# Optimization experiments

Hardware: AMD Instinct MI355X
Metric: run time of the kernel (lower is better)

Reference implementation:

```python
import jax, jax.numpy as jnp
import numpy as np

D_MODEL = 256
POOL = 3
SR = 2  # sampling_ratio
TEMP = 10000.0


def pos_grid(D, H, W):
    """2D sine-cos positional encoding, (D,H,W). pos_y channels first, pos_x second."""
    dq = D // 4
    dim_t = TEMP ** (2.0 * (jnp.arange(dq) // 2).astype(jnp.float32) / dq)

    def enc(coord):  # (L,) -> (L, 2*dq), interleaved sin/cos
        p = coord[:, None] / dim_t
        return jnp.stack([jnp.sin(p), jnp.cos(p)], axis=-1).reshape(coord.shape[0], -1)

    py = enc(jnp.linspace(0.0, 1.0, H))  # (H, 2dq)
    px = enc(jnp.linspace(0.0, 1.0, W))  # (W, 2dq)
    pos = jnp.concatenate([
        jnp.broadcast_to(py[:, None, :], (H, W, 2 * dq)),
        jnp.broadcast_to(px[None, :, :], (H, W, 2 * dq)),
    ], axis=-1)  # (H, W, D)
    return jnp.transpose(pos, (2, 0, 1))  # (D, H, W)


def proj_pos(x, Wp, bp):
    """1x1 conv projection to D then add 2D pos enc. x: (B,C,H,W) -> (B,D,H,W)."""
    y = jnp.einsum('bchw,dc->bdhw', x, Wp) + bp[None, :, None, None]
    return y + pos_grid(Wp.shape[0], x.shape[2], x.shape[3])[None]


def roi_align_mean(feat, bidx, boxes, scale):
    """torchvision roi_align (aligned=True, sampling_ratio=SR, output=POOLxPOOL)
    followed by mean over the pooled grid. feat (B,D,H,W), boxes (N,4) xyxy -> (N,D).
    Since every bin averages SR*SR samples, mean over bins == mean over all samples."""
    B, D, H, W = feat.shape
    f = jnp.transpose(feat, (0, 2, 3, 1))  # (B,H,W,D)
    x1 = boxes[:, 0] * scale - 0.5
    y1 = boxes[:, 1] * scale - 0.5
    x2 = boxes[:, 2] * scale - 0.5
    y2 = boxes[:, 3] * scale - 0.5
    bw = (x2 - x1) / POOL
    bh = (y2 - y1) / POOL
    # sample offsets within roi, in units of bin size: (POOL*SR,)
    off = (jnp.arange(POOL, dtype=jnp.float32)[:, None]
           + (jnp.arange(SR, dtype=jnp.float32)[None, :] + 0.5) / SR).reshape(-1)
    ys = y1[:, None] + bh[:, None] * off  # (N,S) with S = POOL*SR
    xs = x1[:, None] + bw[:, None] * off

    def coords(c, size):
        valid = (c >= -1.0) & (c <= size)
        c = jnp.clip(c, 0.0, None)
        cl = jnp.minimum(jnp.floor(c).astype(jnp.int32), size - 1)
        ch = jnp.minimum(cl + 1, size - 1)
        return cl, ch, c - cl, valid

    yl, yh, ly, vy = coords(ys, H)
    xl, xh, lx, vx = coords(xs, W)
    hy, hx = 1.0 - ly, 1.0 - lx

    def gather(yy, xx):  # -> (N,S,S,D)
        return f[bidx[:, None, None], yy[:, :, None], xx[:, None, :]]

    v = (hy[:, :, None, None] * hx[:, None, :, None] * gather(yl, xl)
         + hy[:, :, None, None] * lx[:, None, :, None] * gather(yl, xh)
         + ly[:, :, None, None] * hx[:, None, :, None] * gather(yh, xl)
         + ly[:, :, None, None] * lx[:, None, :, None] * gather(yh, xh))
    mask = (vy[:, :, None] & vx[:, None, :])[..., None]
    v = jnp.where(mask, v, 0.0)
    return v.mean(axis=(1, 2))  # (N, D)


def token_mlp(tok, ln_g, ln_b, W1, b1, W2, b2):
    m = tok.mean(-1, keepdims=True)
    var = jnp.mean((tok - m) ** 2, -1, keepdims=True)
    h = (tok - m) / jnp.sqrt(var + 1e-5) * ln_g + ln_b
    h = jax.nn.gelu(h @ W1.T + b1, approximate=False)  # torch nn.GELU default = exact
    return h @ W2.T + b2


def setup_inputs():
    key = jax.random.key(0)
    ks = jax.random.split(key, 16)
    B, K, D = 8, 100, D_MODEL
    p3 = jax.random.normal(ks[0], (B, 512, 128, 128), jnp.float32)
    p4 = jax.random.normal(ks[1], (B, 1024, 64, 64), jnp.float32)
    p5 = jax.random.normal(ks[2], (B, 2048, 32, 32), jnp.float32)
    # valid xyxy boxes inside a 1024x1024 frame
    x1 = jax.random.uniform(ks[3], (B, K, 1)) * 880.0
    y1 = jax.random.uniform(ks[4], (B, K, 1)) * 880.0
    bw = jax.random.uniform(ks[5], (B, K, 1)) * 128.0 + 8.0
    bh = jax.random.uniform(ks[6], (B, K, 1)) * 128.0 + 8.0
    boxes = jnp.concatenate([x1, y1, x1 + bw, y1 + bh], axis=-1)

    def lin(k, o, i):
        return (jax.random.normal(k, (o, i), jnp.float32) / np.sqrt(i)).astype(jnp.float32)

    return dict(
        p3=p3, p4=p4, p5=p5, boxes=boxes,
        W3=lin(ks[7], D, 512), b3=jnp.zeros((D,), jnp.float32),
        W4=lin(ks[8], D, 1024), b4=jnp.zeros((D,), jnp.float32),
        W5=lin(ks[9], D, 2048), b5=jnp.zeros((D,), jnp.float32),
        ln_g=jnp.ones((D,), jnp.float32), ln_b=jnp.zeros((D,), jnp.float32),
        W1=lin(ks[10], D, D), b1=jnp.zeros((D,), jnp.float32),
        W2=lin(ks[11], D, D), b2=jnp.zeros((D,), jnp.float32),
        input_w=1024, input_h=1024,
    )


def reference(p3, p4, p5, boxes, W3, b3, W4, b4, W5, b5, ln_g, ln_b, W1, b1, W2, b2, input_w, input_h):
    B, K = boxes.shape[0], boxes.shape[1]
    bidx = jnp.repeat(jnp.arange(B, dtype=jnp.int32), K)  # (B*K,)
    flat = boxes.reshape(-1, 4)
    tok = jnp.zeros((B * K, D_MODEL), jnp.float32)
    for feat, Wp, bp in ((p3, W3, b3), (p4, W4, b4), (p5, W5, b5)):
        y = proj_pos(feat, Wp, bp)
        s = min(y.shape[3] / (input_w + 1e-6), y.shape[2] / (input_h + 1e-6))
        tok = tok + roi_align_mean(y, bidx, flat, s)
    tok = token_mlp(tok, ln_g, ln_b, W1, b1, W2, b2)
    return tok.reshape(B, K, D_MODEL)
```

## Files before the change

### kernel.cpp

```cpp
#include <hip/hip_runtime.h>
#include <math.h>

#ifndef INT_MAX
#define INT_MAX 0x7fffffff
#endif


__device__ __forceinline__ float gelu_exact(float x) {
    return 0.5f * x * (1.0f + erff(x * 0.70710678118654752f));
}

__global__ __launch_bounds__(256)
void build_wt_kernel(const float* __restrict__ W3, const float* __restrict__ W4,
                     const float* __restrict__ W5, const float* __restrict__ W1,
                     const float* __restrict__ W2,
                     float* __restrict__ WT, float* __restrict__ W1T,
                     float* __restrict__ W2T)
{
    int k = blockIdx.x;
    int d = threadIdx.x;
    if (k < 512)       WT[(size_t)k * 256 + d]          = W3[(size_t)d * 512  + k];
    else if (k < 1536) WT[(size_t)k * 256 + d]          = W4[(size_t)d * 1024 + (k - 512)];
    else if (k < 3584) WT[(size_t)k * 256 + d]          = W5[(size_t)d * 2048 + (k - 1536)];
    else if (k < 3840) W1T[(size_t)(k - 3584) * 256 + d] = W1[(size_t)d * 256 + (k - 3584)];
    else               W2T[(size_t)(k - 3840) * 256 + d] = W2[(size_t)d * 256 + (k - 3840)];
}

__global__ __launch_bounds__(256)
void roi_setup_kernel(const float* __restrict__ boxes,
                      const float* __restrict__ b3, const float* __restrict__ b4,
                      const float* __restrict__ b5,
                      const int* __restrict__ iw_p, const int* __restrict__ ih_p,
                      float* __restrict__ WREC, float* __restrict__ P)
{
    const int n   = blockIdx.x;
    const int s   = blockIdx.y;
    const int tid = threadIdx.x;

    int H, W;
    const float* bp;
    if (s == 0)      { H = 128; W = 128; bp = b3; }
    else if (s == 1) { H = 64;  W = 64;  bp = b4; }
    else             { H = 32;  W = 32;  bp = b5; }

    __shared__ float wy[32];
    __shared__ float wx[48];
    __shared__ int   sh_r0, sh_rs, sh_x0, sh_nc;
    __shared__ float sh_syc, sh_sxc;

    if (tid < 32)                 wy[tid]      = 0.0f;
    if (tid >= 32 && tid < 80)    wx[tid - 32] = 0.0f;
    __syncthreads();

    const float scale = fminf((float)W / ((float)(*iw_p) + 1e-6f),
                              (float)H / ((float)(*ih_p) + 1e-6f));

    if (tid == 0) {
        float c1 = boxes[(size_t)n * 4 + 1] * scale - 0.5f;
        float c2 = boxes[(size_t)n * 4 + 3] * scale - 0.5f;
        float bs = (c2 - c1) / 3.0f;
        int   yls[6], yhs[6], vv[6];
        float lys[6];
        int r0 = INT_MAX; float cnt = 0.0f;
        #pragma unroll
        for (int i = 0; i < 6; ++i) {
            float off = 0.25f + 0.5f * (float)i;
            float ys  = c1 + bs * off;
            int v = (ys >= -1.0f) && (ys <= (float)H);
            float yc = fmaxf(ys, 0.0f);
            int yl = (int)floorf(yc); if (yl > H - 1) yl = H - 1;
            int yh = yl + 1;          if (yh > H - 1) yh = H - 1;
            float ly = yc - (float)yl;
            yls[i] = yl; yhs[i] = yh; lys[i] = ly; vv[i] = v;
            if (v) { r0 = min(r0, yl); cnt += 1.0f; }
        }
        if (r0 == INT_MAX) r0 = 0;
        int rmax = 0;
        #pragma unroll
        for (int i = 0; i < 6; ++i) if (vv[i]) {
            int a = min(yls[i] - r0, 31);
            int h = min(yhs[i] - r0, 31);
            wy[a] += 1.0f - lys[i];
            wy[h] += lys[i];
            rmax = max(rmax, h);
        }
        sh_r0 = r0; sh_rs = rmax + 1; sh_syc = cnt;
    }
    if (tid == 1) {
        float c1 = boxes[(size_t)n * 4 + 0] * scale - 0.5f;
        float c2 = boxes[(size_t)n * 4 + 2] * scale - 0.5f;
        float bs = (c2 - c1) / 3.0f;
        int   xls[6], xhs[6], vv[6];
        float lxs[6];
        int x0r = INT_MAX; float cnt = 0.0f;
        #pragma unroll
        for (int i = 0; i < 6; ++i) {
            float off = 0.25f + 0.5f * (float)i;
            float xs  = c1 + bs * off;
            int v = (xs >= -1.0f) && (xs <= (float)W);
            float xc = fmaxf(xs, 0.0f);
            int xl = (int)floorf(xc); if (xl > W - 1) xl = W - 1;
            int xh = xl + 1;          if (xh > W - 1) xh = W - 1;
            float lx = xc - (float)xl;
            xls[i] = xl; xhs[i] = xh; lxs[i] = lx; vv[i] = v;
            if (v) { x0r = min(x0r, xl); cnt += 1.0f; }
        }
        if (x0r == INT_MAX) x0r = 0;
        int x0 = x0r & ~15;
        int imax = 0;
        #pragma unroll
        for (int i = 0; i < 6; ++i) if (vv[i]) {
            int a = min(xls[i] - x0, 47);
            int h = min(xhs[i] - x0, 47);
            wx[a] += 1.0f - lxs[i];
            wx[h] += lxs[i];
            imax = max(imax, h);
        }
        int nc = imax / 16 + 1;
        int ncmax = (W - x0) >> 4;
        nc = min(nc, ncmax);
        sh_x0 = x0; sh_nc = max(nc, 1); sh_sxc = cnt;
    }
    __syncthreads();

    const int r0 = sh_r0, rs = sh_rs, x0 = sh_x0, nc = sh_nc;

    float* rec = &WREC[(size_t)(n * 3 + s) * 96];
    if (tid < 32)                 rec[tid]      = wy[tid];
    else if (tid < 80)            rec[tid]      = wx[tid - 32];
    else if (tid == 80)           rec[80]       = (float)r0;
    else if (tid == 81)           rec[81]       = (float)rs;
    else if (tid == 82)           rec[82]       = (float)x0;
    else if (tid == 83)           rec[83]       = (float)nc;
    else if (tid == 84)           rec[84]       = sh_syc;
    else if (tid == 85)           rec[85]       = sh_sxc;

    {
        const int d = tid;
        const float syc = sh_syc, sxc = sh_sxc;
        float val;
        if (d < 128) {
            int   t     = d >> 2;
            float invf  = expf(-(float)t * (logf(10000.0f) / 32.0f));
            float istep = 1.0f / (float)(H - 1);
            float sum = 0.0f;
            for (int r = 0; r < rs; ++r) {
                float w = wy[r];
                float ang = (float)(r0 + r) * istep * invf;
                float sn, cs; sincosf(ang, &sn, &cs);
                sum = fmaf(w, (d & 1) ? cs : sn, sum);
            }
            val = sxc * sum;
        } else {
            int   d2    = d - 128;
            int   t     = d2 >> 2;
            float invf  = expf(-(float)t * (logf(10000.0f) / 32.0f));
            float istep = 1.0f / (float)(W - 1);
            float sum = 0.0f;
            int nx = nc << 4;
            for (int j = 0; j < nx; ++j) {
                float w = wx[j];
                if (w != 0.0f) {
                    float ang = (float)(x0 + j) * istep * invf;
                    float sn, cs; sincosf(ang, &sn, &cs);
                    sum = fmaf(w, (d & 1) ? cs : sn, sum);
                }
            }
            val = syc * sum;
        }
        float cnt = syc * sxc;
        P[((size_t)n * 3 + s) * 256 + d] = (val + cnt * bp[d]) * (1.0f / 36.0f);
    }
}

__global__ __launch_bounds__(256)
void roi_gather_kernel(const float* __restrict__ p3, const float* __restrict__ p4,
                       const float* __restrict__ p5,
                       const float* __restrict__ WREC,
                       float* __restrict__ G, int K)
{
    const int yc  = blockIdx.x;
    const int n   = blockIdx.y;
    const int tid = threadIdx.x;

    int s, chunk;
    if (yc < 8)       { s = 0; chunk = yc; }
    else if (yc < 24) { s = 1; chunk = yc - 8; }
    else              { s = 2; chunk = yc - 24; }

    int C, H, W, koff;
    const float* feat;
    if (s == 0)      { C = 512;  H = 128; W = 128; koff = 0;    feat = p3; }
    else if (s == 1) { C = 1024; H = 64;  W = 64;  koff = 512;  feat = p4; }
    else             { C = 2048; H = 32;  W = 32;  koff = 1536; feat = p5; }
    const int HW = H * W;
    const int b  = n / K;

    __shared__ float sh[96];
    if (tid < 96) sh[tid] = WREC[(size_t)(n * 3 + s) * 96 + tid];
    __syncthreads();

    const int r0 = (int)sh[80];
    const int rs = (int)sh[81];
    const int x0 = (int)sh[82];
    const int nc = (int)sh[83];

    const int c    = chunk * 64 + (tid >> 2);
    const int slot = tid & 3;

    const float* fp = feat + (size_t)b * C * HW + (size_t)c * HW
                    + (size_t)r0 * W + x0 + slot * 4;

    float acc = 0.0f;
    for (int ch = 0; ch < nc; ++ch) {
        const float4 wxv = *(const float4*)&sh[32 + (ch << 4) + slot * 4];
        const float* a = fp + (ch << 4);
        float4 ra = make_float4(0.f, 0.f, 0.f, 0.f);
        int r = 0;
        for (; r + 4 <= rs; r += 4) {
            const float4 v0 = *(const float4*)(a + (size_t)(r + 0) * W);
            const float4 v1 = *(const float4*)(a + (size_t)(r + 1) * W);
            const float4 v2 = *(const float4*)(a + (size_t)(r + 2) * W);
            const float4 v3 = *(const float4*)(a + (size_t)(r + 3) * W);
            const float w0 = sh[r], w1 = sh[r + 1], w2 = sh[r + 2], w3 = sh[r + 3];
            ra.x = fmaf(w0, v0.x, ra.x); ra.y = fmaf(w0, v0.y, ra.y);
            ra.z = fmaf(w0, v0.z, ra.z); ra.w = fmaf(w0, v0.w, ra.w);
            ra.x = fmaf(w1, v1.x, ra.x); ra.y = fmaf(w1, v1.y, ra.y);
            ra.z = fmaf(w1, v1.z, ra.z); ra.w = fmaf(w1, v1.w, ra.w);
            ra.x = fmaf(w2, v2.x, ra.x); ra.y = fmaf(w2, v2.y, ra.y);
            ra.z = fmaf(w2, v2.z, ra.z); ra.w = fmaf(w2, v2.w, ra.w);
            ra.x = fmaf(w3, v3.x, ra.x); ra.y = fmaf(w3, v3.y, ra.y);
            ra.z = fmaf(w3, v3.z, ra.z); ra.w = fmaf(w3, v3.w, ra.w);
        }
        for (; r < rs; ++r) {
            const float4 v = *(const float4*)(a + (size_t)r * W);
            const float w = sh[r];
            ra.x = fmaf(w, v.x, ra.x); ra.y = fmaf(w, v.y, ra.y);
            ra.z = fmaf(w, v.z, ra.z); ra.w = fmaf(w, v.w, ra.w);
        }
        float d = ra.x * wxv.x + ra.y * wxv.y + ra.z * wxv.z + ra.w * wxv.w;
        acc += d;
    }
    acc += __shfl_xor(acc, 1, 4);
    acc += __shfl_xor(acc, 2, 4);
    if (slot == 0)
        G[(size_t)n * 3584 + koff + c] = acc * (1.0f / 36.0f);
}

__global__ __launch_bounds__(256)
void proj_gemm_kernel(const float* __restrict__ G, const float* __restrict__ WT,
                      float* __restrict__ part, int N)
{
    const int n0  = blockIdx.x * 8;
    const int kc  = blockIdx.y;
    const int tid = threadIdx.x;

    __shared__ float gl[8][128];
    float acc[8];
    #pragma unroll
    for (int t = 0; t < 8; ++t) acc[t] = 0.0f;

    const int kbase = kc * 512;
    const int lt  = tid >> 5;
    const int lc  = (tid & 31) * 4;

    for (int sub = 0; sub < 4; ++sub) {
        const float4 g4 = *(const float4*)&G[(size_t)(n0 + lt) * 3584 + kbase + sub * 128 + lc];
        *(float4*)&gl[lt][lc] = g4;
        __syncthreads();
        const float* wtp = &WT[(size_t)(kbase + sub * 128) * 256 + tid];
        #pragma unroll 4
        for (int k = 0; k < 128; ++k) {
            float w = wtp[(size_t)k * 256];
            #pragma unroll
            for (int t = 0; t < 8; ++t) acc[t] = fmaf(gl[t][k], w, acc[t]);
        }
        __syncthreads();
    }
    #pragma unroll
    for (int t = 0; t < 8; ++t)
        part[((size_t)kc * N + n0 + t) * 256 + tid] = acc[t];
}

__global__ __launch_bounds__(256)
void mlp_kernel(const float* __restrict__ part, const float* __restrict__ P,
                const float* __restrict__ lng, const float* __restrict__ lnb,
                const float* __restrict__ W1T, const float* __restrict__ b1,
                const float* __restrict__ W2T, const float* __restrict__ b2,
                float* __restrict__ out, int N)
{
    const int n0  = blockIdx.x * 8;
    const int tid = threadIdx.x;

    __shared__ float tokl[8][257];
    __shared__ float hl[8][257];
    __shared__ float mval[8], rstd[8];

    #pragma unroll
    for (int t = 0; t < 8; ++t) {
        const int n = n0 + t;
        float v = 0.0f;
        #pragma unroll
        for (int c = 0; c < 7; ++c) v += part[((size_t)c * N + n) * 256 + tid];
        #pragma unroll
        for (int s = 0; s < 3; ++s) v += P[((size_t)n * 3 + s) * 256 + tid];
        tokl[t][tid] = v;
    }
    __syncthreads();

    const int wv = tid >> 6, lane = tid & 63;
    for (int t = wv; t < 8; t += 4) {
        float x0 = tokl[t][lane], x1 = tokl[t][lane + 64];
        float x2 = tokl[t][lane + 128], x3 = tokl[t][lane + 192];
        float sm = x0 + x1 + x2 + x3;
        float sq = x0 * x0 + x1 * x1 + x2 * x2 + x3 * x3;
        #pragma unroll
        for (int o = 32; o; o >>= 1) { sm += __shfl_xor(sm, o); sq += __shfl_xor(sq, o); }
        if (lane == 0) {
            float m   = sm * (1.0f / 256.0f);
            float var = sq * (1.0f / 256.0f) - m * m;
            mval[t] = m;
            rstd[t] = rsqrtf(var + 1e-5f);
        }
    }
    __syncthreads();

    const float g = lng[tid], be = lnb[tid];
    #pragma unroll
    for (int t = 0; t < 8; ++t)
        hl[t][tid] = (tokl[t][tid] - mval[t]) * rstd[t] * g + be;
    __syncthreads();

    float acc[8];
    const float bb1 = b1[tid];
    #pragma unroll
    for (int t = 0; t < 8; ++t) acc[t] = bb1;
    for (int k = 0; k < 256; ++k) {
        float w = W1T[(size_t)k * 256 + tid];
        #pragma unroll
        for (int t = 0; t < 8; ++t) acc[t] = fmaf(hl[t][k], w, acc[t]);
    }
    __syncthreads();
    #pragma unroll
    for (int t = 0; t < 8; ++t) tokl[t][tid] = gelu_exact(acc[t]);
    __syncthreads();

    const float bb2 = b2[tid];
    #pragma unroll
    for (int t = 0; t < 8; ++t) acc[t] = bb2;
    for (int k = 0; k < 256; ++k) {
        float w = W2T[(size_t)k * 256 + tid];
        #pragma unroll
        for (int t = 0; t < 8; ++t) acc[t] = fmaf(tokl[t][k], w, acc[t]);
    }
    #pragma unroll
    for (int t = 0; t < 8; ++t)
        out[(size_t)(n0 + t) * 256 + tid] = acc[t];
}

extern "C" void kernel_launch(void* const* d_in, const int* in_sizes, int n_in,
                              void* d_out, int out_size, void* d_ws, size_t ws_size,
                              hipStream_t stream)
{
    const float* p3    = (const float*)d_in[0];
    const float* p4    = (const float*)d_in[1];
    const float* p5    = (const float*)d_in[2];
    const float* boxes = (const float*)d_in[3];
    const float* W3    = (const float*)d_in[4];
    const float* b3    = (const float*)d_in[5];
    const float* W4    = (const float*)d_in[6];
    const float* b4    = (const float*)d_in[7];
    const float* W5    = (const float*)d_in[8];
    const float* b5    = (const float*)d_in[9];
    const float* lng   = (const float*)d_in[10];
    const float* lnb   = (const float*)d_in[11];
    const float* W1    = (const float*)d_in[12];
    const float* b1    = (const float*)d_in[13];
    const float* W2    = (const float*)d_in[14];
    const float* b2    = (const float*)d_in[15];
    const int*   iw    = (const int*)d_in[16];
    const int*   ih    = (const int*)d_in[17];

    const int B = in_sizes[0] / (512 * 128 * 128);
    const int N = out_size / 256;
    const int K = N / B;

    float* G    = (float*)d_ws;
    float* P    = G + (size_t)N * 3584;
    float* WT   = P + (size_t)N * 3 * 256;
    float* W1T  = WT + (size_t)3584 * 256;
    float* W2T  = W1T + (size_t)256 * 256;
    float* part = W2T + (size_t)256 * 256;
    float* WREC = part + (size_t)7 * N * 256;

    float* out = (float*)d_out;

    build_wt_kernel<<<4096, 256, 0, stream>>>(W3, W4, W5, W1, W2, WT, W1T, W2T);
    roi_setup_kernel<<<dim3(N, 3), 256, 0, stream>>>(boxes, b3, b4, b5, iw, ih, WREC, P);
    roi_gather_kernel<<<dim3(56, N), 256, 0, stream>>>(p3, p4, p5, WREC, G, K);
    proj_gemm_kernel<<<dim3(N / 8, 7), 256, 0, stream>>>(G, WT, part, N);
    mlp_kernel<<<N / 8, 256, 0, stream>>>(part, P, lng, lnb, W1T, b1, W2T, b2, out, N);
}
```

Measured before the change: 269.7 us.

## Project full feature maps with fp16 MFMA before ROI sampling

Reorders the pipeline: each pyramid level is first projected to 256 channels with an fp16 MFMA GEMM over all pixels, and bilinear ROI sampling then runs on the compact fp16 projected maps. Positional encoding and bias are handled analytically in a setup kernel. This replaces the gather over wide 512–2048 channel inputs and the per-ROI projection GEMM with dense tensor-core work. It adds full-map compute and fp16 rounding, and falls back to the old path if the workspace is too small.

```diff
diff --git a/kernel.cpp b/kernel.cpp
--- a/kernel.cpp
+++ b/kernel.cpp
@@ -1,14 +1,421 @@
 #include <hip/hip_runtime.h>
+#include <hip/hip_fp16.h>
 #include <math.h>
 
 #ifndef INT_MAX
 #define INT_MAX 0x7fffffff
 #endif
 
+typedef __attribute__((ext_vector_type(8))) _Float16 f16x8;
+typedef __attribute__((ext_vector_type(4))) float   f32x4;
+
 
 __device__ __forceinline__ float gelu_exact(float x) {
     return 0.5f * x * (1.0f + erff(x * 0.70710678118654752f));
 }
+
+
+__global__ __launch_bounds__(256)
+void build_wt2_kernel(const float* __restrict__ W3, const float* __restrict__ W4,
+                      const float* __restrict__ W5, const float* __restrict__ W1,
+                      const float* __restrict__ W2,
+                      __half* __restrict__ WTD,
+                      float* __restrict__ W1T, float* __restrict__ W2T)
+{
+    const int k = blockIdx.x;
+    const int d = threadIdx.x;
+    if (k < 3584) {
+        const size_t i = (size_t)k * 256 + d;
+        float v;
+        if (i < 131072)       v = W3[i];
+        else if (i < 393216)  v = W4[i - 131072];
+        else                  v = W5[i - 393216];
+        WTD[i] = __float2half(v);
+    } else if (k < 3840) {
+        W1T[(size_t)(k - 3584) * 256 + d] = W1[(size_t)d * 256 + (k - 3584)];
+    } else {
+        W2T[(size_t)(k - 3840) * 256 + d] = W2[(size_t)d * 256 + (k - 3840)];
+    }
+}
+
+__global__ __launch_bounds__(256)
+void roi_setup2_kernel(const float* __restrict__ boxes,
+                       const float* __restrict__ b3, const float* __restrict__ b4,
+                       const float* __restrict__ b5,
+                       const int* __restrict__ iw_p, const int* __restrict__ ih_p,
+                       float* __restrict__ SREC, float* __restrict__ P)
+{
+    const int n   = blockIdx.x;
+    const int s   = blockIdx.y;
+    const int tid = threadIdx.x;
+
+    int H, W;
+    const float* bp;
+    if (s == 0)      { H = 128; W = 128; bp = b3; }
+    else if (s == 1) { H = 64;  W = 64;  bp = b4; }
+    else             { H = 32;  W = 32;  bp = b5; }
+
+    __shared__ float wy[32];
+    __shared__ float wx[48];
+    __shared__ int   sh_r0, sh_rs, sh_x0, sh_xs;
+    __shared__ float sh_syc, sh_sxc;
+
+    if (tid < 32)              wy[tid]      = 0.0f;
+    if (tid >= 32 && tid < 80) wx[tid - 32] = 0.0f;
+    __syncthreads();
+
+    const float scale = fminf((float)W / ((float)(*iw_p) + 1e-6f),
+                              (float)H / ((float)(*ih_p) + 1e-6f));
+    float* rec = &SREC[(size_t)(n * 3 + s) * 64];
+
+    if (tid == 0) {
+        float c1 = boxes[(size_t)n * 4 + 1] * scale - 0.5f;
+        float c2 = boxes[(size_t)n * 4 + 3] * scale - 0.5f;
+        float bs = (c2 - c1) / 3.0f;
+        int   yls[6], yhs[6], vv[6];
+        float lys[6];
+        int r0 = INT_MAX; float cnt = 0.0f;
+        #pragma unroll
+        for (int i = 0; i < 6; ++i) {
+            float off = 0.25f + 0.5f * (float)i;
+            float ys  = c1 + bs * off;
+            int v = (ys >= -1.0f) && (ys <= (float)H);
+            float yc = fmaxf(ys, 0.0f);
+            int yl = (int)floorf(yc); if (yl > H - 1) yl = H - 1;
+            int yh = yl + 1;          if (yh > H - 1) yh = H - 1;
+            float ly = yc - (float)yl;
+            yls[i] = yl; yhs[i] = yh; lys[i] = ly; vv[i] = v;
+            if (v) { r0 = min(r0, yl); cnt += 1.0f; }
+        }
+        if (r0 == INT_MAX) r0 = 0;
+        int rmax = 0;
+        #pragma unroll
+        for (int i = 0; i < 6; ++i) if (vv[i]) {
+            int a = min(yls[i] - r0, 31);
+            int h = min(yhs[i] - r0, 31);
+            wy[a] += 1.0f - lys[i];
+            wy[h] += lys[i];
+            rmax = max(rmax, h);
+        }
+        sh_r0 = r0; sh_rs = rmax + 1; sh_syc = cnt;
+        int cntn = 0;
+        for (int r = 0; r <= rmax && cntn < 12; ++r) {
+            if (wy[r] != 0.0f) {
+                rec[4 + cntn]  = (float)(r0 + r);
+                rec[16 + cntn] = wy[r];
+                ++cntn;
+            }
+        }
+        rec[0] = (float)cntn;
+        rec[2] = cnt;
+    }
+    if (tid == 1) {
+        float c1 = boxes[(size_t)n * 4 + 0] * scale - 0.5f;
+        float c2 = boxes[(size_t)n * 4 + 2] * scale - 0.5f;
+        float bs = (c2 - c1) / 3.0f;
+        int   xls[6], xhs[6], vv[6];
+        float lxs[6];
+        int x0r = INT_MAX; float cnt = 0.0f;
+        #pragma unroll
+        for (int i = 0; i < 6; ++i) {
+            float off = 0.25f + 0.5f * (float)i;
+            float xs  = c1 + bs * off;
+            int v = (xs >= -1.0f) && (xs <= (float)W);
+            float xc = fmaxf(xs, 0.0f);
+            int xl = (int)floorf(xc); if (xl > W - 1) xl = W - 1;
+            int xh = xl + 1;          if (xh > W - 1) xh = W - 1;
+            float lx = xc - (float)xl;
+            xls[i] = xl; xhs[i] = xh; lxs[i] = lx; vv[i] = v;
+            if (v) { x0r = min(x0r, xl); cnt += 1.0f; }
+        }
+        if (x0r == INT_MAX) x0r = 0;
+        int imax = 0;
+        #pragma unroll
+        for (int i = 0; i < 6; ++i) if (vv[i]) {
+            int a = min(xls[i] - x0r, 47);
+            int h = min(xhs[i] - x0r, 47);
+            wx[a] += 1.0f - lxs[i];
+            wx[h] += lxs[i];
+            imax = max(imax, h);
+        }
+        sh_x0 = x0r; sh_xs = imax + 1; sh_sxc = cnt;
+        int cntn = 0;
+        for (int j = 0; j <= imax && cntn < 12; ++j) {
+            if (wx[j] != 0.0f) {
+                rec[28 + cntn] = (float)(x0r + j);
+                rec[40 + cntn] = wx[j];
+                ++cntn;
+            }
+        }
+        rec[1] = (float)cntn;
+        rec[3] = cnt;
+    }
+    __syncthreads();
+
+    const int r0 = sh_r0, rs = sh_rs, x0 = sh_x0, xsr = sh_xs;
+
+    {
+        const int d = tid;
+        const float syc = sh_syc, sxc = sh_sxc;
+        float val;
+        if (d < 128) {
+            int   t     = d >> 2;
+            float invf  = expf(-(float)t * (logf(10000.0f) / 32.0f));
+            float istep = 1.0f / (float)(H - 1);
+            float sum = 0.0f;
+            for (int r = 0; r < rs; ++r) {
+                float w = wy[r];
+                if (w != 0.0f) {
+                    float ang = (float)(r0 + r) * istep * invf;
+                    float sn, cs; sincosf(ang, &sn, &cs);
+                    sum = fmaf(w, (d & 1) ? cs : sn, sum);
+                }
+            }
+            val = sxc * sum;
+        } else {
+            int   d2    = d - 128;
+            int   t     = d2 >> 2;
+            float invf  = expf(-(float)t * (logf(10000.0f) / 32.0f));
+            float istep = 1.0f / (float)(W - 1);
+            float sum = 0.0f;
+            for (int j = 0; j < xsr; ++j) {
+                float w = wx[j];
+                if (w != 0.0f) {
+                    float ang = (float)(x0 + j) * istep * invf;
+                    float sn, cs; sincosf(ang, &sn, &cs);
+                    sum = fmaf(w, (d & 1) ? cs : sn, sum);
+                }
+            }
+            val = syc * sum;
+        }
+        float cnt = syc * sxc;
+        P[((size_t)n * 3 + s) * 256 + d] = (val + cnt * bp[d]) * (1.0f / 36.0f);
+    }
+}
+
+__global__ __launch_bounds__(256, 2)
+void proj_kernel(const float* __restrict__ p3, const float* __restrict__ p4,
+                 const float* __restrict__ p5,
+                 const __half* __restrict__ wt3, const __half* __restrict__ wt4,
+                 const __half* __restrict__ wt5,
+                 __half* __restrict__ F3, __half* __restrict__ F4,
+                 __half* __restrict__ F5,
+                 int n5, int n4)
+{
+    int bid = blockIdx.x;
+    const float* feat; const __half* wt; __half* F;
+    int C, HW, m0;
+    if (bid < n5)            { C = 2048; HW = 1024;  feat = p5; wt = wt5; F = F5; m0 = bid * 128; }
+    else if (bid < n5 + n4)  { C = 1024; HW = 4096;  feat = p4; wt = wt4; F = F4; m0 = (bid - n5) * 128; }
+    else                     { C = 512;  HW = 16384; feat = p3; wt = wt3; F = F3; m0 = (bid - n5 - n4) * 128; }
+
+    const int tid = threadIdx.x;
+    const int wv  = tid >> 6;
+    const int l   = tid & 63;
+    const int lm  = l & 15;
+    const int lg  = l >> 4;
+    const int b    = m0 / HW;
+    const int pos0 = m0 % HW;
+    const int K = C, nk = K >> 5;
+
+    __shared__ __half wlds[2][256 * 40];
+
+    const float* a0p = feat + (size_t)b * C * HW + pos0 + wv * 32 + lm;
+    const float* a1p = a0p + 16;
+
+    f32x4 acc[32];
+    #pragma unroll
+    for (int i = 0; i < 32; ++i) acc[i] = (f32x4){0.f, 0.f, 0.f, 0.f};
+
+    float ar0[8], ar1[8], an0[8], an1[8];
+    #pragma unroll
+    for (int j = 0; j < 8; ++j) {
+        const size_t ko = (size_t)(lg * 8 + j) * HW;
+        ar0[j] = a0p[ko]; ar1[j] = a1p[ko];
+    }
+    #pragma unroll
+    for (int it = 0; it < 4; ++it) {
+        const int slot = tid + it * 256;
+        const int d = slot >> 2, kq = slot & 3;
+        const uint4 w = *(const uint4*)(wt + (size_t)d * K + kq * 8);
+        *(uint4*)&wlds[0][d * 40 + kq * 8] = w;
+    }
+    __syncthreads();
+
+    for (int t = 0; t < nk; ++t) {
+        const int cur = t & 1;
+        const bool more = (t + 1 < nk);
+        uint4 ws[4];
+        if (more) {
+            const int k0n = (t + 1) * 32;
+            #pragma unroll
+            for (int j = 0; j < 8; ++j) {
+                const size_t ko = (size_t)(k0n + lg * 8 + j) * HW;
+                an0[j] = a0p[ko]; an1[j] = a1p[ko];
+            }
+            const __half* wsrc = wt + k0n;
+            #pragma unroll
+            for (int it = 0; it < 4; ++it) {
+                const int slot = tid + it * 256;
+                const int d = slot >> 2, kq = slot & 3;
+                ws[it] = *(const uint4*)(wsrc + (size_t)d * K + kq * 8);
+            }
+        }
+        f16x8 af0, af1;
+        #pragma unroll
+        for (int j = 0; j < 8; ++j) {
+            af0[j] = (_Float16)ar0[j];
+            af1[j] = (_Float16)ar1[j];
+        }
+        #pragma unroll
+        for (int nt = 0; nt < 16; ++nt) {
+            const f16x8 bf = *(const f16x8*)&wlds[cur][(nt * 16 + lm) * 40 + lg * 8];
+            acc[nt]      = __builtin_amdgcn_mfma_f32_16x16x32_f16(af0, bf, acc[nt], 0, 0, 0);
+            acc[nt + 16] = __builtin_amdgcn_mfma_f32_16x16x32_f16(af1, bf, acc[nt + 16], 0, 0, 0);
+        }
+        if (more) {
+            #pragma unroll
+            for (int it = 0; it < 4; ++it) {
+                const int slot = tid + it * 256;
+                const int d = slot >> 2, kq = slot & 3;
+                *(uint4*)&wlds[cur ^ 1][d * 40 + kq * 8] = ws[it];
+            }
+            #pragma unroll
+            for (int j = 0; j < 8; ++j) { ar0[j] = an0[j]; ar1[j] = an1[j]; }
+        }
+        __syncthreads();
+    }
+
+    #pragma unroll
+    for (int mt = 0; mt < 2; ++mt) {
+        #pragma unroll
+        for (int nt = 0; nt < 16; ++nt) {
+            #pragma unroll
+            for (int i = 0; i < 4; ++i) {
+                const int px = pos0 + wv * 32 + mt * 16 + lg * 4 + i;
+                F[((size_t)b * HW + px) * 256 + nt * 16 + lm] =
+                    __float2half(acc[nt + mt * 16][i]);
+            }
+        }
+    }
+}
+
+__global__ __launch_bounds__(256)
+void sample_kernel(const __half* __restrict__ F3, const __half* __restrict__ F4,
+                   const __half* __restrict__ F5,
+                   const float* __restrict__ SREC, const float* __restrict__ P,
+                   float* __restrict__ tok, int K100)
+{
+    const int n   = blockIdx.x;
+    const int d   = threadIdx.x;
+    const int b   = n / K100;
+
+    __shared__ float rsh[3][64];
+    if (d < 64)            rsh[0][d]       = SREC[(size_t)(n * 3 + 0) * 64 + d];
+    else if (d < 128)      rsh[1][d - 64]  = SREC[(size_t)(n * 3 + 1) * 64 + (d - 64)];
+    else if (d < 192)      rsh[2][d - 128] = SREC[(size_t)(n * 3 + 2) * 64 + (d - 128)];
+    __syncthreads();
+
+    float acc = 0.0f;
+    #pragma unroll
+    for (int s = 0; s < 3; ++s) {
+        const __half* F; int HW, W;
+        if (s == 0)      { F = F3; HW = 16384; W = 128; }
+        else if (s == 1) { F = F4; HW = 4096;  W = 64; }
+        else             { F = F5; HW = 1024;  W = 32; }
+        const float* rec = rsh[s];
+        const int ny = (int)rec[0];
+        const int nx = (int)rec[1];
+        const size_t base = (size_t)b * HW * 256 + d;
+        for (int i = 0; i < ny; ++i) {
+            const int   row = (int)rec[4 + i];
+            const float wyv = rec[16 + i];
+            const size_t rb = base + (size_t)(row * W) * 256;
+            float rsum = 0.0f;
+            for (int j = 0; j < nx; ++j) {
+                const int   col = (int)rec[28 + j];
+                const float wxv = rec[40 + j];
+                rsum = fmaf(wxv, __half2float(F[rb + (size_t)col * 256]), rsum);
+            }
+            acc = fmaf(wyv, rsum, acc);
+        }
+    }
+    acc = acc * (1.0f / 36.0f)
+        + P[((size_t)n * 3 + 0) * 256 + d]
+        + P[((size_t)n * 3 + 1) * 256 + d]
+        + P[((size_t)n * 3 + 2) * 256 + d];
+    tok[(size_t)n * 256 + d] = acc;
+}
+
+__global__ __launch_bounds__(256)
+void mlp2_kernel(const float* __restrict__ tok,
+                 const float* __restrict__ lng, const float* __restrict__ lnb,
+                 const float* __restrict__ W1T, const float* __restrict__ b1,
+                 const float* __restrict__ W2T, const float* __restrict__ b2,
+                 float* __restrict__ out, int N)
+{
+    const int n0  = blockIdx.x * 8;
+    const int tid = threadIdx.x;
+
+    __shared__ float tokl[8][257];
+    __shared__ float hl[8][257];
+    __shared__ float mval[8], rstd[8];
+
+    #pragma unroll
+    for (int t = 0; t < 8; ++t)
+        tokl[t][tid] = tok[(size_t)(n0 + t) * 256 + tid];
+    __syncthreads();
+
+    const int wv = tid >> 6, lane = tid & 63;
+    for (int t = wv; t < 8; t += 4) {
+        float x0 = tokl[t][lane], x1 = tokl[t][lane + 64];
+        float x2 = tokl[t][lane + 128], x3 = tokl[t][lane + 192];
+        float sm = x0 + x1 + x2 + x3;
+        float sq = x0 * x0 + x1 * x1 + x2 * x2 + x3 * x3;
+        #pragma unroll
+        for (int o = 32; o; o >>= 1) { sm += __shfl_xor(sm, o); sq += __shfl_xor(sq, o); }
+        if (lane == 0) {
+            float m   = sm * (1.0f / 256.0f);
+            float var = sq * (1.0f / 256.0f) - m * m;
+            mval[t] = m;
+            rstd[t] = rsqrtf(var + 1e-5f);
+        }
+    }
+    __syncthreads();
+
+    const float g = lng[tid], be = lnb[tid];
+    #pragma unroll
+    for (int t = 0; t < 8; ++t)
+        hl[t][tid] = (tokl[t][tid] - mval[t]) * rstd[t] * g + be;
+    __syncthreads();
+
+    float acc[8];
+    const float bb1 = b1[tid];
+    #pragma unroll
+    for (int t = 0; t < 8; ++t) acc[t] = bb1;
+    for (int k = 0; k < 256; ++k) {
+        float w = W1T[(size_t)k * 256 + tid];
+        #pragma unroll
+        for (int t = 0; t < 8; ++t) acc[t] = fmaf(hl[t][k], w, acc[t]);
+    }
+    __syncthreads();
+    #pragma unroll
+    for (int t = 0; t < 8; ++t) tokl[t][tid] = gelu_exact(acc[t]);
+    __syncthreads();
+
+    const float bb2 = b2[tid];
+    #pragma unroll
+    for (int t = 0; t < 8; ++t) acc[t] = bb2;
+    for (int k = 0; k < 256; ++k) {
+        float w = W2T[(size_t)k * 256 + tid];
+        #pragma unroll
+        for (int t = 0; t < 8; ++t) acc[t] = fmaf(tokl[t][k], w, acc[t]);
+    }
+    #pragma unroll
+    for (int t = 0; t < 8; ++t)
+        out[(size_t)(n0 + t) * 256 + tid] = acc[t];
+}
+
 
 __global__ __launch_bounds__(256)
 void build_wt_kernel(const float* __restrict__ W3, const float* __restrict__ W4,
@@ -238,8 +645,8 @@
             ra.x = fmaf(w, v.x, ra.x); ra.y = fmaf(w, v.y, ra.y);
             ra.z = fmaf(w, v.z, ra.z); ra.w = fmaf(w, v.w, ra.w);
         }
-        float d = ra.x * wxv.x + ra.y * wxv.y + ra.z * wxv.z + ra.w * wxv.w;
-        acc += d;
+        float dsum = ra.x * wxv.x + ra.y * wxv.y + ra.z * wxv.z + ra.w * wxv.w;
+        acc += dsum;
     }
     acc += __shfl_xor(acc, 1, 4);
     acc += __shfl_xor(acc, 2, 4);
@@ -383,21 +790,59 @@
 
     const int B = in_sizes[0] / (512 * 128 * 128);
     const int N = out_size / 256;
-    const int K = N / B;
-
-    float* G    = (float*)d_ws;
-    float* P    = G + (size_t)N * 3584;
-    float* WT   = P + (size_t)N * 3 * 256;
-    float* W1T  = WT + (size_t)3584 * 256;
-    float* W2T  = W1T + (size_t)256 * 256;
-    float* part = W2T + (size_t)256 * 256;
-    float* WREC = part + (size_t)7 * N * 256;
+    const int K100 = N / B;
 
     float* out = (float*)d_out;
 
-    build_wt_kernel<<<4096, 256, 0, stream>>>(W3, W4, W5, W1, W2, WT, W1T, W2T);
-    roi_setup_kernel<<<dim3(N, 3), 256, 0, stream>>>(boxes, b3, b4, b5, iw, ih, WREC, P);
-    roi_gather_kernel<<<dim3(56, N), 256, 0, stream>>>(p3, p4, p5, WREC, G, K);
-    proj_gemm_kernel<<<dim3(N / 8, 7), 256, 0, stream>>>(G, WT, part, N);
-    mlp_kernel<<<N / 8, 256, 0, stream>>>(part, P, lng, lnb, W1T, b1, W2T, b2, out, N);
-}
+    const size_t szF3   = (size_t)B * 16384 * 256 * 2;
+    const size_t szF4   = (size_t)B * 4096  * 256 * 2;
+    const size_t szF5   = (size_t)B * 1024  * 256 * 2;
+    const size_t szWTD  = (size_t)3584 * 256 * 2;
+    const size_t szSREC = (size_t)N * 3 * 64 * 4;
+    const size_t szP    = (size_t)N * 3 * 256 * 4;
+    const size_t szTok  = (size_t)N * 256 * 4;
+    const size_t szWT12 = (size_t)256 * 256 * 4;
+    const size_t need_new = szF3 + szF4 + szF5 + szWTD + szSREC + szP + szTok + 2 * szWT12;
+
+    if (ws_size >= need_new) {
+        char* w = (char*)d_ws;
+        __half* F3   = (__half*)w;            w += szF3;
+        __half* F4   = (__half*)w;            w += szF4;
+        __half* F5   = (__half*)w;            w += szF5;
+        __half* WTD  = (__half*)w;            w += szWTD;
+        float*  SREC = (float*)w;             w += szSREC;
+        float*  P    = (float*)w;             w += szP;
+        float*  tok  = (float*)w;             w += szTok;
+        float*  W1T  = (float*)w;             w += szWT12;
+        float*  W2T  = (float*)w;             w += szWT12;
+
+        const __half* wt3 = WTD;
+        const __half* wt4 = WTD + 131072;
+        const __half* wt5 = WTD + 393216;
+
+        const int n5 = B * 8;
+        const int n4 = B * 32;
+        const int n3 = B * 128;
+
+        build_wt2_kernel<<<4096, 256, 0, stream>>>(W3, W4, W5, W1, W2, WTD, W1T, W2T);
+        roi_setup2_kernel<<<dim3(N, 3), 256, 0, stream>>>(boxes, b3, b4, b5, iw, ih, SREC, P);
+        proj_kernel<<<n5 + n4 + n3, 256, 0, stream>>>(p3, p4, p5, wt3, wt4, wt5,
+                                                      F3, F4, F5, n5, n4);
+        sample_kernel<<<N, 256, 0, stream>>>(F3, F4, F5, SREC, P, tok, K100);
+        mlp2_kernel<<<N / 8, 256, 0, stream>>>(tok, lng, lnb, W1T, b1, W2T, b2, out, N);
+    } else {
+        float* G    = (float*)d_ws;
+        float* P    = G + (size_t)N * 3584;
+        float* WT   = P + (size_t)N * 3 * 256;
+        float* W1T  = WT + (size_t)3584 * 256;
+        float* W2T  = W1T + (size_t)256 * 256;
+        float* part = W2T + (size_t)256 * 256;
+        float* WREC = part + (size_t)7 * N * 256;
+
+        build_wt_kernel<<<4096, 256, 0, stream>>>(W3, W4, W5, W1, W2, WT, W1T, W2T);
+        roi_setup_kernel<<<dim3(N, 3), 256, 0, stream>>>(boxes, b3, b4, b5, iw, ih, WREC, P);
+        roi_gather_kernel<<<dim3(56, N), 256, 0, stream>>>(p3, p4, p5, WREC, G, K100);
+        proj_gemm_kernel<<<dim3(N / 8, 7), 256, 0, stream>>>(G, WT, part, N);
+        mlp_kernel<<<N / 8, 256, 0, stream>>>(part, P, lng, lnb, W1T, b1, W2T, b2, out, N);
+    }
+}
```

After: 393.3 us. 45.8% more time.
